# Optimization experiments

Measured on AMD Instinct MI355X. Metric: run time of the kernel, lower is better.

The kernel has to match this reference:

```python
import jax, jax.numpy as jnp
import numpy as np

NUM_HEADS = 16


def setup_inputs() -> dict:
    key = jax.random.key(0)
    ks = jax.random.split(key, 5)
    S, B, N, C = 4, 2, 2048, 1024
    return {
        "x_all": jax.random.normal(ks[0], (S, B, N, C), dtype=jnp.float32),
        "w_qkv": jax.random.normal(ks[1], (C, 3 * C), dtype=jnp.float32) * (C ** -0.5),
        "b_qkv": jax.random.normal(ks[2], (3 * C,), dtype=jnp.float32) * 0.02,
        "w_proj": jax.random.normal(ks[3], (C, C), dtype=jnp.float32) * (C ** -0.5),
        "b_proj": jax.random.normal(ks[4], (C,), dtype=jnp.float32) * 0.02,
    }


def reference(x_all, w_qkv, b_qkv, w_proj, b_proj):
    # x_all: [S, B, N, C] -- S = cp_dim ring shards, each rank holds [B, N, C]
    S, B, N, C = x_all.shape
    H = NUM_HEADS
    D = C // H
    scale = 1.0 / np.sqrt(D).astype(np.float32)

    # same qkv projection on every rank
    qkv = (jnp.einsum("sbnc,ce->sbne", x_all, w_qkv) + b_qkv)
    qkv = qkv.reshape(S, B, N, 3, H, D)
    # rank 0's queries: [B, H, N, D]
    q = jnp.transpose(qkv[0, :, :, 0], (0, 2, 1, 3))
    # all shards' keys/values: [S, B, H, N, D]
    k = jnp.transpose(qkv[:, :, :, 1], (0, 1, 3, 2, 4))
    v = jnp.transpose(qkv[:, :, :, 2], (0, 1, 3, 2, 4))

    # ring loop: online softmax merge across KV shards (numerically stable
    # form of the source's exp(lse)-weighted average)
    attn_out, lse = None, None
    for s in range(S):
        scores = jnp.einsum("bhnd,bhmd->bhnm", q, k[s]) * scale  # [B,H,N,N]
        new_lse = jax.nn.logsumexp(scores, axis=-1)               # [B,H,N]
        probs = jnp.exp(scores - new_lse[..., None])
        new_out = jnp.einsum("bhnm,bhmd->bhnd", probs, v[s])      # [B,H,N,D]
        if attn_out is None:
            attn_out, lse = new_out, new_lse
        else:
            m = jnp.logaddexp(lse, new_lse)
            attn_out = (attn_out * jnp.exp(lse - m)[..., None]
                        + new_out * jnp.exp(new_lse - m)[..., None])
            lse = m

    # [B,H,N,D] -> [B,N,C]
    out = jnp.transpose(attn_out, (0, 2, 1, 3)).reshape(B, N, C)
    return out @ w_proj + b_proj
```

## Files before the change

kernel.cpp:

```cpp
#include <hip/hip_runtime.h>
#include <hip/hip_bf16.h>


typedef __bf16 bf16x8 __attribute__((ext_vector_type(8)));
typedef float v4f __attribute__((ext_vector_type(4)));

#if __has_builtin(__builtin_amdgcn_exp2f)
#define EXP2F(x) __builtin_amdgcn_exp2f(x)
#else
#define EXP2F(x) exp2f(x)
#endif

__device__ __forceinline__ float bf2f(unsigned short h) {
  union { unsigned int u; float f; } a; a.u = ((unsigned int)h) << 16; return a.f;
}
__device__ __forceinline__ unsigned short f2bf(float f) {
  union { float f; unsigned int u; } a; a.f = f;
  unsigned int u = a.u;
  unsigned int r = (u + 0x7fffu + ((u >> 16) & 1u)) >> 16;
  return (unsigned short)r;
}
__device__ __forceinline__ unsigned int pack2t(float a, float b) {
  union { float f; unsigned int u; } ua, ub; ua.f = a; ub.f = b;
  return (ua.u >> 16) | (ub.u & 0xffff0000u);
}
__device__ __forceinline__ bf16x8 ldfrag16(const unsigned short* p) {
  union { uint4 u; bf16x8 v; } x; x.u = *(const uint4*)p; return x.v;
}
__device__ __forceinline__ bf16x8 ones8() {
  union { unsigned short s[8]; bf16x8 v; } x;
#pragma unroll
  for (int i = 0; i < 8; i++) x.s[i] = 0x3F80;
  return x.v;
}
__device__ __forceinline__ void gld_lds16(const unsigned short* g, unsigned short* l) {
  __builtin_amdgcn_global_load_lds((__attribute__((address_space(1))) void*)g,
                                   (__attribute__((address_space(3))) void*)l, 16, 0, 0);
}

__global__ void detect_dtype(const unsigned short* __restrict__ x, int* flag) {
  __shared__ int cnt;
  if (threadIdx.x == 0) cnt = 0;
  __syncthreads();
  int sane = 0;
#pragma unroll
  for (int j = 0; j < 4; j++) {
    unsigned short v = x[2 * (threadIdx.x + 64 * j)];
    int e = (v >> 7) & 0xFF;
    if (e >= 90 && e <= 140) sane++;
  }
  atomicAdd(&cnt, sane);
  __syncthreads();
  if (threadIdx.x == 0) *flag = (cnt > 160) ? 0 : 1;
}

__global__ void conv_to_bf16(const void* __restrict__ in, unsigned short* __restrict__ out,
                             int n4, const int* __restrict__ flag) {
  int i = blockIdx.x * blockDim.x + threadIdx.x;
  if (i >= n4) return;
  if (*flag) {
    float4 v = ((const float4*)in)[i];
    ushort4 o;
    o.x = f2bf(v.x); o.y = f2bf(v.y); o.z = f2bf(v.z); o.w = f2bf(v.w);
    ((ushort4*)out)[i] = o;
  } else {
    ((ushort4*)out)[i] = ((const ushort4*)in)[i];
  }
}

__global__ void conv_bias(const void* __restrict__ bq_in, const void* __restrict__ bp_in,
                          unsigned short* __restrict__ bq, unsigned short* __restrict__ bp,
                          const int* __restrict__ flag) {
  int i = blockIdx.x * 256 + threadIdx.x;
  const void* in = (i < 768) ? bq_in : bp_in;
  unsigned short* out = (i < 768) ? bq : bp;
  int j = (i < 768) ? i : i - 768;
  if (*flag) {
    float4 v = ((const float4*)in)[j];
    ushort4 o;
    o.x = f2bf(v.x); o.y = f2bf(v.y); o.z = f2bf(v.z); o.w = f2bf(v.w);
    ((ushort4*)out)[j] = o;
  } else {
    ((ushort4*)out)[j] = ((const ushort4*)in)[j];
  }
}

__global__ void trans_both(const void* __restrict__ wqkv, const void* __restrict__ wproj,
                           unsigned short* __restrict__ wt1, unsigned short* __restrict__ wt2,
                           const int* __restrict__ flag) {
  __shared__ unsigned short t[32][33];
  int tx = threadIdx.x, ty = threadIdx.y;
  int bx = blockIdx.x;
  const void* in; unsigned short* out; int C, c0;
  if (bx < 96) { in = wqkv; out = wt1; C = 3072; c0 = bx * 32; }
  else         { in = wproj; out = wt2; C = 1024; c0 = (bx - 96) * 32; }
  const int R = 1024;
  int r0 = blockIdx.y * 32;
  int fp = *flag;
#pragma unroll
  for (int j = 0; j < 32; j += 8) {
    unsigned short v;
    if (fp) v = f2bf(((const float*)in)[(r0 + ty + j) * C + c0 + tx]);
    else    v = ((const unsigned short*)in)[(r0 + ty + j) * C + c0 + tx];
    t[ty + j][tx] = v;
  }
  __syncthreads();
#pragma unroll
  for (int j = 0; j < 32; j += 8) out[(c0 + ty + j) * R + r0 + tx] = t[tx][ty + j];
}

template <int MODE>
__launch_bounds__(256, 3)
__global__ void gemm_bt(const unsigned short* __restrict__ A,
                        const unsigned short* __restrict__ Bt,
                        const unsigned short* __restrict__ bias,
                        void* __restrict__ Cout,
                        int K, int ldc, const int* __restrict__ flag,
                        const unsigned short* Bt2, const unsigned short* bias2,
                        void* Cout2) {
  __shared__ unsigned short As[128 * 32];
  __shared__ unsigned short Bs[128 * 32];
  int tid = threadIdx.x;
  int w = tid >> 6, lane = tid & 63, col = lane & 15, quad = lane >> 4;
  int wm = w >> 1, wn = w & 1;
  int n0 = blockIdx.x * 128;
  int m0 = blockIdx.y * 128;
  const unsigned short* Bt_ = Bt;
  const unsigned short* bias_ = bias;
  void* Cout_ = Cout;
  bool isq = false;
  if constexpr (MODE == 3) {
    if (blockIdx.y >= 128) {
      m0 = (blockIdx.y - 128) * 128;
      Bt_ = Bt2; bias_ = bias2; Cout_ = Cout2;
      isq = true;
    }
  }
  int fp = 0;
  if constexpr (MODE == 2) fp = *flag;

  v4f acc[4][4];
#pragma unroll
  for (int i = 0; i < 4; i++)
#pragma unroll
    for (int j = 0; j < 4; j++) acc[i][j] = v4f{0.f, 0.f, 0.f, 0.f};

  int ra0 = tid >> 2, cc = tid & 3;
  const unsigned short* ga0 = &A[(m0 + ra0) * K + cc * 8];
  const unsigned short* ga1 = ga0 + 64 * K;
  const unsigned short* gb0 = &Bt_[(n0 + ra0) * K + cc * 8];
  const unsigned short* gb1 = gb0 + 64 * K;
  unsigned short* lA0 = &As[(w * 16) * 32];
  unsigned short* lA1 = &As[(64 + w * 16) * 32];
  unsigned short* lB0 = &Bs[(w * 16) * 32];
  unsigned short* lB1 = &Bs[(64 + w * 16) * 32];

  int niter = K >> 5;
  for (int it = 0; it < niter; it++) {
    __syncthreads();
    gld_lds16(ga0, lA0); gld_lds16(ga1, lA1);
    gld_lds16(gb0, lB0); gld_lds16(gb1, lB1);
    ga0 += 32; ga1 += 32; gb0 += 32; gb1 += 32;
    __syncthreads();
    bf16x8 af[4], bfr[4];
#pragma unroll
    for (int mi = 0; mi < 4; mi++) af[mi] = ldfrag16(&As[(wm * 64 + mi * 16 + col) * 32 + quad * 8]);
#pragma unroll
    for (int ni = 0; ni < 4; ni++) bfr[ni] = ldfrag16(&Bs[(wn * 64 + ni * 16 + col) * 32 + quad * 8]);
#pragma unroll
    for (int mi = 0; mi < 4; mi++)
#pragma unroll
      for (int ni = 0; ni < 4; ni++)
        acc[mi][ni] = __builtin_amdgcn_mfma_f32_16x16x32_bf16(af[mi], bfr[ni], acc[mi][ni], 0, 0, 0);
  }

  float bv[4];
#pragma unroll
  for (int ni = 0; ni < 4; ni++) bv[ni] = bf2f(bias_[n0 + wn * 64 + ni * 16 + col]);

  if constexpr (MODE == 1) {
    int rgb0 = m0 + wm * 64;
    int s = rgb0 >> 12, b = (rgb0 >> 11) & 1, n = rgb0 & 2047;
    int kvg0 = s * 2048 + n;
#pragma unroll
    for (int ni = 0; ni < 4; ni++) {
      int cg = n0 + wn * 64 + ni * 16 + col;
      int h = cg >> 6, d = cg & 63;
      unsigned short* rowp = &((unsigned short*)Cout_)[((b * 16 + h) * 64 + d) * 8192 + kvg0];
      float bvn = bv[ni];
#pragma unroll
      for (int r = 0; r < 4; r++) {
        ushort4 o;
        o.x = f2bf(acc[0][ni][r] + bvn);
        o.y = f2bf(acc[1][ni][r] + bvn);
        o.z = f2bf(acc[2][ni][r] + bvn);
        o.w = f2bf(acc[3][ni][r] + bvn);
        *(ushort4*)&rowp[4 * (quad * 4 + r)] = o;
      }
    }
  } else {
#pragma unroll
    for (int mi = 0; mi < 4; mi++)
#pragma unroll
      for (int ni = 0; ni < 4; ni++) {
        float vals[4];
#pragma unroll
        for (int r = 0; r < 4; r++) vals[r] = acc[mi][ni][r] + bv[ni];
        if constexpr (MODE == 3) {
          if (isq) {
#pragma unroll
            for (int r = 0; r < 4; r++) vals[r] *= 0.1803368801111601f;
          }
        }
        int rgb = m0 + wm * 64 + mi * 16 + quad * 4;
        int cg  = n0 + wn * 64 + ni * 16 + col;
        if constexpr (MODE == 0 || MODE == 3) {
          unsigned short* C = (unsigned short*)Cout_;
#pragma unroll
          for (int r = 0; r < 4; r++) C[(rgb + r) * ldc + cg] = f2bf(vals[r]);
        } else {
          if (fp) {
            float* C = (float*)Cout_;
#pragma unroll
            for (int r = 0; r < 4; r++) C[(rgb + r) * ldc + cg] = vals[r];
          } else {
            unsigned short* C = (unsigned short*)Cout_;
#pragma unroll
            for (int r = 0; r < 4; r++) C[(rgb + r) * ldc + cg] = f2bf(vals[r]);
          }
        }
      }
  }
}

__launch_bounds__(512, 4)
__global__ void attn_kernel(const unsigned short* __restrict__ qbuf,
                            const unsigned short* __restrict__ kbuf,
                            const unsigned short* __restrict__ vt,
                            float* __restrict__ po,
                            float* __restrict__ lbuf) {
  __shared__ unsigned short QP[256 * 64];
  __shared__ unsigned short Ks[2][64 * 64];
  __shared__ unsigned short Vs[2][64 * 64];
  int tid = threadIdx.x;
  int w = tid >> 6, lane = tid & 63, col = lane & 15, quad = lane >> 4;
  int id = blockIdx.x;
  int xcd = id & 7, slot = id >> 3;
  int qt = slot & 7, gsub = slot >> 3;
  int g = gsub * 8 + xcd;
  int bh = g >> 1, half = g & 1;
  int b = bh >> 4, h = bh & 15;
  int q0 = qt * 256;

#pragma unroll
  for (int i = 0; i < 4; i++) {
    int s2 = tid + 512 * i; int r = s2 >> 3; int c = s2 & 7;
    *(uint4*)&QP[r * 64 + 8 * (c ^ (r & 7))] =
        *(const uint4*)&qbuf[(b * 2048 + q0 + r) * 1024 + h * 64 + c * 8];
  }

  int r0 = tid >> 3, c0 = tid & 7;
  const unsigned short* kp = &kbuf[((half * 2) * 4096 + b * 2048 + r0) * 1024 + h * 64 + c0 * 8];
  const unsigned short* vp = &vt[(bh * 64 + r0) * 8192 + half * 4096 + c0 * 8];
  int sdst = r0 * 64 + 8 * (c0 ^ (r0 & 7));
  {
    uint4 k0 = *(const uint4*)kp, v0 = *(const uint4*)vp;
    *(uint4*)&Ks[0][sdst] = k0;
    *(uint4*)&Vs[0][sdst] = v0;
  }

  __syncthreads();
  bf16x8 aQ[2][2];
#pragma unroll
  for (int mi = 0; mi < 2; mi++)
#pragma unroll
    for (int kk = 0; kk < 2; kk++) {
      int row = w * 32 + mi * 16 + col;
      aQ[mi][kk] = ldfrag16(&QP[row * 64 + 8 * ((kk * 4 + quad) ^ (col & 7))]);
    }

  unsigned short* Ps = &QP[w * 32 * 64];

  const bf16x8 vone = ones8();
  v4f o[2][4];
  v4f acc_l[2] = {v4f{0.f, 0.f, 0.f, 0.f}, v4f{0.f, 0.f, 0.f, 0.f}};
#pragma unroll
  for (int mi = 0; mi < 2; mi++)
#pragma unroll
    for (int di = 0; di < 4; di++) o[mi][di] = v4f{0.f, 0.f, 0.f, 0.f};

  for (int kvt = 0; kvt < 64; kvt++) {
    int p = kvt & 1;
    uint4 pk, pv;
    if (kvt < 63) {
      int kstep = (((kvt + 1) & 31) == 0) ? (2048 + 64) * 1024 : 64 * 1024;
      kp += kstep; vp += 64;
      pk = *(const uint4*)kp; pv = *(const uint4*)vp;
    }

    v4f sc[2][4];
#pragma unroll
    for (int mi = 0; mi < 2; mi++)
#pragma unroll
      for (int ni = 0; ni < 4; ni++) sc[mi][ni] = v4f{0.f, 0.f, 0.f, 0.f};
#pragma unroll
    for (int kk = 0; kk < 2; kk++) {
      bf16x8 bK[4];
#pragma unroll
      for (int ni = 0; ni < 4; ni++) {
        int row = ni * 16 + col;
        bK[ni] = ldfrag16(&Ks[p][row * 64 + 8 * ((kk * 4 + quad) ^ (col & 7))]);
      }
#pragma unroll
      for (int mi = 0; mi < 2; mi++)
#pragma unroll
        for (int ni = 0; ni < 4; ni++)
          sc[mi][ni] = __builtin_amdgcn_mfma_f32_16x16x32_bf16(aQ[mi][kk], bK[ni], sc[mi][ni], 0, 0, 0);
    }

#pragma unroll
    for (int mi = 0; mi < 2; mi++)
#pragma unroll
      for (int ni = 0; ni < 4; ni++)
#pragma unroll
        for (int r = 0; r < 4; r++) sc[mi][ni][r] = EXP2F(sc[mi][ni][r]);

#pragma unroll
    for (int mi = 0; mi < 2; mi++)
#pragma unroll
      for (int r = 0; r < 4; r++) {
        unsigned int dw0 = pack2t(sc[mi][0][r], sc[mi][1][r]);
        unsigned int dw1 = pack2t(sc[mi][2][r], sc[mi][3][r]);
        int pr = mi * 16 + quad * 4 + r;
        *(uint2*)&Ps[pr * 64 + ((col * 4) ^ ((pr & 7) * 8))] = uint2{dw0, dw1};
      }

    if (kvt < 63) {
      *(uint4*)&Ks[p ^ 1][sdst] = pk;
      *(uint4*)&Vs[p ^ 1][sdst] = pv;
    }

#pragma unroll
    for (int kk = 0; kk < 2; kk++) {
      bf16x8 aP[2];
#pragma unroll
      for (int mi = 0; mi < 2; mi++) {
        int row = mi * 16 + col;
        aP[mi] = ldfrag16(&Ps[row * 64 + 8 * ((kk * 4 + quad) ^ (col & 7))]);
        acc_l[mi] = __builtin_amdgcn_mfma_f32_16x16x32_bf16(aP[mi], vone, acc_l[mi], 0, 0, 0);
      }
      bf16x8 bV[4];
#pragma unroll
      for (int di = 0; di < 4; di++) {
        int row = di * 16 + col;
        bV[di] = ldfrag16(&Vs[p][row * 64 + 8 * ((kk * 4 + quad) ^ (col & 7))]);
      }
#pragma unroll
      for (int mi = 0; mi < 2; mi++)
#pragma unroll
        for (int di = 0; di < 4; di++)
          o[mi][di] = __builtin_amdgcn_mfma_f32_16x16x32_bf16(aP[mi], bV[di], o[mi][di], 0, 0, 0);
    }

    __syncthreads();
  }

  float* pb = po + half * 4194304;
#pragma unroll
  for (int mi = 0; mi < 2; mi++)
#pragma unroll
    for (int r = 0; r < 4; r++) {
      int n = q0 + w * 32 + mi * 16 + quad * 4 + r;
      if (col == 0) lbuf[half * 65536 + (b * 16 + h) * 2048 + n] = acc_l[mi][r];
#pragma unroll
      for (int di = 0; di < 4; di++) {
        int c = h * 64 + di * 16 + col;
        pb[(b * 2048 + n) * 1024 + c] = o[mi][di][r];
      }
    }
}

__global__ void merge_halves(const float* __restrict__ po, const float* __restrict__ lbuf,
                             unsigned short* __restrict__ attn) {
  int i = blockIdx.x * 256 + threadIdx.x;
  int r = i >> 8, c4 = i & 255;
  float l = lbuf[((r >> 11) * 16 + (c4 >> 4)) * 2048 + (r & 2047)] +
            lbuf[65536 + ((r >> 11) * 16 + (c4 >> 4)) * 2048 + (r & 2047)];
  float inv = 1.f / l;
  float4 a = ((const float4*)po)[i];
  float4 b = ((const float4*)po)[1048576 + i];
  ushort4 o;
  o.x = f2bf((a.x + b.x) * inv); o.y = f2bf((a.y + b.y) * inv);
  o.z = f2bf((a.z + b.z) * inv); o.w = f2bf((a.w + b.w) * inv);
  ((ushort4*)attn)[i] = o;
}

extern "C" void kernel_launch(void* const* d_in, const int* in_sizes, int n_in,
                              void* d_out, int out_size, void* d_ws, size_t ws_size,
                              hipStream_t stream) {
  const void* x      = d_in[0];
  const void* w_qkv  = d_in[1];
  const void* b_qkv  = d_in[2];
  const void* w_proj = d_in[3];
  const void* b_proj = d_in[4];

  char* ws = (char*)d_ws;
  unsigned short* xb   = (unsigned short*)(ws);
  unsigned short* kk   = (unsigned short*)(ws + 33554432);
  unsigned short* vt   = (unsigned short*)(ws + 67108864);
  unsigned short* q0b  = (unsigned short*)(ws + 100663296);
  unsigned short* attn = (unsigned short*)(ws + 109051904);
  unsigned short* wt1  = (unsigned short*)(ws + 117440512);
  unsigned short* wt2  = (unsigned short*)(ws + 123731968);
  unsigned short* bq   = (unsigned short*)(ws + 125829120);
  unsigned short* bp   = (unsigned short*)(ws + 125835264);
  int* flag            = (int*)(ws + 125837312);
  float* po   = (float*)xb;
  float* lbuf = (float*)wt1;

  detect_dtype<<<1, 64, 0, stream>>>((const unsigned short*)x, flag);

  conv_to_bf16<<<16384, 256, 0, stream>>>(x, xb, 4194304, flag);
  conv_bias<<<4, 256, 0, stream>>>(b_qkv, b_proj, bq, bp, flag);
  trans_both<<<dim3(128, 32), dim3(32, 8), 0, stream>>>(w_qkv, w_proj, wt1, wt2, flag);

  gemm_bt<3><<<dim3(8, 160), 256, 0, stream>>>(xb, wt1 + 1024 * 1024, bq + 1024, kk,
                                               1024, 1024, flag, wt1, bq, q0b);
  gemm_bt<1><<<dim3(8, 128), 256, 0, stream>>>(xb, wt1 + 2048 * 1024, bq + 2048, vt,
                                               1024, 0, flag, nullptr, nullptr, nullptr);

  attn_kernel<<<512, 512, 0, stream>>>(q0b, kk, vt, po, lbuf);
  merge_halves<<<4096, 256, 0, stream>>>(po, lbuf, attn);

  gemm_bt<2><<<dim3(8, 32), 256, 0, stream>>>(attn, wt2, bp, d_out,
                                              1024, 1024, flag, nullptr, nullptr, nullptr);
}
```

Before: 327.9 us.

## Compute transposed scores so P stays in registers, skipping LDS round trip

The QK^T MFMA now computes S^T (K as the A operand, Q as B), so each lane's exp'd scores already sit in the A-fragment layout needed by the PV MFMA and can be packed straight into bf16 registers. This removes the P write/read through shared memory and the Q staging buffer in LDS. Q fragments are loaded directly from global memory. The V-transpose writer in the QKV GEMM permutes the kv index order to match the new P column ordering. LDS footprint drops, which may raise occupancy, at the cost of an interleaved V layout that must stay consistent between the GEMM and the attention kernel.

Result: faster. 318.0 us (-3.0%).

```diff
diff --git a/kernel.cpp b/kernel.cpp
--- a/kernel.cpp
+++ b/kernel.cpp
@@ -190,12 +190,13 @@
       float bvn = bv[ni];
 #pragma unroll
       for (int r = 0; r < 4; r++) {
-        ushort4 o;
-        o.x = f2bf(acc[0][ni][r] + bvn);
-        o.y = f2bf(acc[1][ni][r] + bvn);
-        o.z = f2bf(acc[2][ni][r] + bvn);
-        o.w = f2bf(acc[3][ni][r] + bvn);
-        *(ushort4*)&rowp[4 * (quad * 4 + r)] = o;
+        ushort2 e, o2;
+        e.x = f2bf(acc[0][ni][r] + bvn);
+        e.y = f2bf(acc[2][ni][r] + bvn);
+        o2.x = f2bf(acc[1][ni][r] + bvn);
+        o2.y = f2bf(acc[3][ni][r] + bvn);
+        *(ushort2*)&rowp[2 * (quad * 4 + r)] = e;
+        *(ushort2*)&rowp[32 + 2 * (quad * 4 + r)] = o2;
       }
     }
   } else {
@@ -239,7 +240,6 @@
                             const unsigned short* __restrict__ vt,
                             float* __restrict__ po,
                             float* __restrict__ lbuf) {
-  __shared__ unsigned short QP[256 * 64];
   __shared__ unsigned short Ks[2][64 * 64];
   __shared__ unsigned short Vs[2][64 * 64];
   int tid = threadIdx.x;
@@ -252,12 +252,13 @@
   int b = bh >> 4, h = bh & 15;
   int q0 = qt * 256;
 
-#pragma unroll
-  for (int i = 0; i < 4; i++) {
-    int s2 = tid + 512 * i; int r = s2 >> 3; int c = s2 & 7;
-    *(uint4*)&QP[r * 64 + 8 * (c ^ (r & 7))] =
-        *(const uint4*)&qbuf[(b * 2048 + q0 + r) * 1024 + h * 64 + c * 8];
-  }
+  bf16x8 aQ[2][2];
+#pragma unroll
+  for (int mj = 0; mj < 2; mj++)
+#pragma unroll
+    for (int kk = 0; kk < 2; kk++)
+      aQ[mj][kk] = ldfrag16(&qbuf[(b * 2048 + q0 + w * 32 + mj * 16 + col) * 1024 +
+                                  h * 64 + kk * 32 + quad * 8]);
 
   int r0 = tid >> 3, c0 = tid & 7;
   const unsigned short* kp = &kbuf[((half * 2) * 4096 + b * 2048 + r0) * 1024 + h * 64 + c0 * 8];
@@ -269,25 +270,15 @@
     *(uint4*)&Vs[0][sdst] = v0;
   }
 
-  __syncthreads();
-  bf16x8 aQ[2][2];
-#pragma unroll
-  for (int mi = 0; mi < 2; mi++)
-#pragma unroll
-    for (int kk = 0; kk < 2; kk++) {
-      int row = w * 32 + mi * 16 + col;
-      aQ[mi][kk] = ldfrag16(&QP[row * 64 + 8 * ((kk * 4 + quad) ^ (col & 7))]);
-    }
-
-  unsigned short* Ps = &QP[w * 32 * 64];
-
   const bf16x8 vone = ones8();
   v4f o[2][4];
   v4f acc_l[2] = {v4f{0.f, 0.f, 0.f, 0.f}, v4f{0.f, 0.f, 0.f, 0.f}};
 #pragma unroll
-  for (int mi = 0; mi < 2; mi++)
-#pragma unroll
-    for (int di = 0; di < 4; di++) o[mi][di] = v4f{0.f, 0.f, 0.f, 0.f};
+  for (int mj = 0; mj < 2; mj++)
+#pragma unroll
+    for (int di = 0; di < 4; di++) o[mj][di] = v4f{0.f, 0.f, 0.f, 0.f};
+
+  __syncthreads();
 
   for (int kvt = 0; kvt < 64; kvt++) {
     int p = kvt & 1;
@@ -298,41 +289,43 @@
       pk = *(const uint4*)kp; pv = *(const uint4*)vp;
     }
 
-    v4f sc[2][4];
-#pragma unroll
-    for (int mi = 0; mi < 2; mi++)
-#pragma unroll
-      for (int ni = 0; ni < 4; ni++) sc[mi][ni] = v4f{0.f, 0.f, 0.f, 0.f};
+    v4f sc[4][2];
+#pragma unroll
+    for (int ni = 0; ni < 4; ni++)
+#pragma unroll
+      for (int mj = 0; mj < 2; mj++) sc[ni][mj] = v4f{0.f, 0.f, 0.f, 0.f};
 #pragma unroll
     for (int kk = 0; kk < 2; kk++) {
-      bf16x8 bK[4];
+      bf16x8 aK[4];
 #pragma unroll
       for (int ni = 0; ni < 4; ni++) {
         int row = ni * 16 + col;
-        bK[ni] = ldfrag16(&Ks[p][row * 64 + 8 * ((kk * 4 + quad) ^ (col & 7))]);
-      }
-#pragma unroll
-      for (int mi = 0; mi < 2; mi++)
-#pragma unroll
-        for (int ni = 0; ni < 4; ni++)
-          sc[mi][ni] = __builtin_amdgcn_mfma_f32_16x16x32_bf16(aQ[mi][kk], bK[ni], sc[mi][ni], 0, 0, 0);
-    }
-
-#pragma unroll
-    for (int mi = 0; mi < 2; mi++)
+        aK[ni] = ldfrag16(&Ks[p][row * 64 + 8 * ((kk * 4 + quad) ^ (col & 7))]);
+      }
 #pragma unroll
       for (int ni = 0; ni < 4; ni++)
 #pragma unroll
-        for (int r = 0; r < 4; r++) sc[mi][ni][r] = EXP2F(sc[mi][ni][r]);
-
-#pragma unroll
-    for (int mi = 0; mi < 2; mi++)
-#pragma unroll
-      for (int r = 0; r < 4; r++) {
-        unsigned int dw0 = pack2t(sc[mi][0][r], sc[mi][1][r]);
-        unsigned int dw1 = pack2t(sc[mi][2][r], sc[mi][3][r]);
-        int pr = mi * 16 + quad * 4 + r;
-        *(uint2*)&Ps[pr * 64 + ((col * 4) ^ ((pr & 7) * 8))] = uint2{dw0, dw1};
+        for (int mj = 0; mj < 2; mj++)
+          sc[ni][mj] = __builtin_amdgcn_mfma_f32_16x16x32_bf16(aK[ni], aQ[mj][kk], sc[ni][mj], 0, 0, 0);
+    }
+
+#pragma unroll
+    for (int ni = 0; ni < 4; ni++)
+#pragma unroll
+      for (int mj = 0; mj < 2; mj++)
+#pragma unroll
+        for (int r = 0; r < 4; r++) sc[ni][mj][r] = EXP2F(sc[ni][mj][r]);
+
+    bf16x8 aP[2][2];
+#pragma unroll
+    for (int mj = 0; mj < 2; mj++)
+#pragma unroll
+      for (int kk = 0; kk < 2; kk++) {
+        union { unsigned int d[4]; bf16x8 v; } u;
+#pragma unroll
+        for (int t = 0; t < 4; t++)
+          u.d[t] = pack2t(sc[kk][mj][t], sc[kk + 2][mj][t]);
+        aP[mj][kk] = u.v;
       }
 
     if (kvt < 63) {
@@ -342,13 +335,9 @@
 
 #pragma unroll
     for (int kk = 0; kk < 2; kk++) {
-      bf16x8 aP[2];
-#pragma unroll
-      for (int mi = 0; mi < 2; mi++) {
-        int row = mi * 16 + col;
-        aP[mi] = ldfrag16(&Ps[row * 64 + 8 * ((kk * 4 + quad) ^ (col & 7))]);
-        acc_l[mi] = __builtin_amdgcn_mfma_f32_16x16x32_bf16(aP[mi], vone, acc_l[mi], 0, 0, 0);
-      }
+#pragma unroll
+      for (int mj = 0; mj < 2; mj++)
+        acc_l[mj] = __builtin_amdgcn_mfma_f32_16x16x32_bf16(aP[mj][kk], vone, acc_l[mj], 0, 0, 0);
       bf16x8 bV[4];
 #pragma unroll
       for (int di = 0; di < 4; di++) {
@@ -356,10 +345,10 @@
         bV[di] = ldfrag16(&Vs[p][row * 64 + 8 * ((kk * 4 + quad) ^ (col & 7))]);
       }
 #pragma unroll
-      for (int mi = 0; mi < 2; mi++)
+      for (int mj = 0; mj < 2; mj++)
 #pragma unroll
         for (int di = 0; di < 4; di++)
-          o[mi][di] = __builtin_amdgcn_mfma_f32_16x16x32_bf16(aP[mi], bV[di], o[mi][di], 0, 0, 0);
+          o[mj][di] = __builtin_amdgcn_mfma_f32_16x16x32_bf16(aP[mj][kk], bV[di], o[mj][di], 0, 0, 0);
     }
 
     __syncthreads();
@@ -367,15 +356,15 @@
 
   float* pb = po + half * 4194304;
 #pragma unroll
-  for (int mi = 0; mi < 2; mi++)
+  for (int mj = 0; mj < 2; mj++)
 #pragma unroll
     for (int r = 0; r < 4; r++) {
-      int n = q0 + w * 32 + mi * 16 + quad * 4 + r;
-      if (col == 0) lbuf[half * 65536 + (b * 16 + h) * 2048 + n] = acc_l[mi][r];
+      int n = q0 + w * 32 + mj * 16 + quad * 4 + r;
+      if (col == 0) lbuf[half * 65536 + (b * 16 + h) * 2048 + n] = acc_l[mj][r];
 #pragma unroll
       for (int di = 0; di < 4; di++) {
         int c = h * 64 + di * 16 + col;
-        pb[(b * 2048 + n) * 1024 + c] = o[mi][di][r];
+        pb[(b * 2048 + n) * 1024 + c] = o[mj][di][r];
       }
     }
 }
```
